# Performance work log

Measured on AMD Instinct MI355X. Metric: run time of the kernel, lower is better.

Reference implementation:

```python
import jax, jax.numpy as jnp
import numpy as np

N, D, H, C, L, G, E = 50000, 128, 128, 40, 3, 4, 800000
GRID = jnp.linspace(-2.0, 2.0, G)          # RBF grid on [-2, 2]
DENOM = 4.0 / (G - 1)                      # (grid_max - grid_min) / (num_grids - 1)


def _layernorm(x, g, b, eps=1e-5):
    m = x.mean(-1, keepdims=True)
    v = x.var(-1, keepdims=True)
    return (x - m) * jax.lax.rsqrt(v + eps) * g + b


def _fkan(x, ln_g, ln_b, sw, bw, bb):
    # FastKANLayer: layernorm -> Gaussian RBF basis -> bias-free spline linear, + silu base update
    xn = _layernorm(x, ln_g, ln_b)
    basis = jnp.exp(-(((xn[..., None] - GRID) / DENOM) ** 2))     # [n, d, G]
    ret = basis.reshape(x.shape[0], -1) @ sw.T                    # [n, out]
    return ret + jax.nn.silu(x) @ bw.T + bb


def _gcn_prop(h, src, dst, n):
    # symmetric GCN normalization with self-loops already appended to src/dst
    deg = jax.ops.segment_sum(jnp.ones(src.shape[0], h.dtype), dst, num_segments=n)
    dis = jnp.where(deg > 0, jax.lax.rsqrt(deg), 0.0)
    norm = dis[src] * dis[dst]                                    # [e]
    return jax.ops.segment_sum(h[src] * norm[:, None], dst, num_segments=n)


def _batchnorm(x, g, b, eps=1e-5):
    m = x.mean(0)
    v = x.var(0)  # biased variance, as torch BN uses for normalization
    return (x - m) * jax.lax.rsqrt(v + eps) * g + b


def setup_inputs() -> dict:
    key = jax.random.key(0)
    ks = jax.random.split(key, 8)
    x = jax.random.normal(ks[0], (N, D), jnp.float32)
    edge_index = jax.random.randint(ks[1], (2, E), 0, N, jnp.int64)
    return {
        "x": x,
        "edge_index": edge_index,
        "ln_g": jnp.ones((L, D), jnp.float32),
        "ln_b": jnp.zeros((L, D), jnp.float32),
        "sw": jax.random.normal(ks[2], (L, H, D * G), jnp.float32) * 0.1,
        "bw": jax.random.normal(ks[3], (L, H, D), jnp.float32) * (1.0 / np.sqrt(D)),
        "bb": jnp.zeros((L, H), jnp.float32),
        "gcn_bias": jnp.zeros((L, H), jnp.float32),
        "bn_g": jnp.ones((L, H), jnp.float32),
        "bn_b": jnp.zeros((L, H), jnp.float32),
        "ln_g_out": jnp.ones((D + L * H,), jnp.float32),
        "ln_b_out": jnp.zeros((D + L * H,), jnp.float32),
        "sw_out": jax.random.normal(ks[4], (C, (D + L * H) * G), jnp.float32) * 0.1,
        "bw_out": jax.random.normal(ks[5], (C, D + L * H), jnp.float32) * (1.0 / np.sqrt(D + L * H)),
        "bb_out": jnp.zeros((C,), jnp.float32),
    }


def reference(x, edge_index, ln_g, ln_b, sw, bw, bb, gcn_bias, bn_g, bn_b,
              ln_g_out, ln_b_out, sw_out, bw_out, bb_out):
    loops = jnp.arange(N, dtype=edge_index.dtype)
    src = jnp.concatenate([edge_index[0], loops])
    dst = jnp.concatenate([edge_index[1], loops])
    feats = [x]
    h = x
    for i in range(L):  # fixed small layer count
        h = _fkan(h, ln_g[i], ln_b[i], sw[i], bw[i], bb[i])
        h = _gcn_prop(h, src, dst, N) + gcn_bias[i]
        h = _batchnorm(h, bn_g[i], bn_b[i])
        feats.append(h)
    xcat = jnp.concatenate(feats, axis=1)  # [N, D + L*H] skip-concat
    return _fkan(xcat, ln_g_out, ln_b_out, sw_out, bw_out, bb_out)
```

## Files before the change

### kernel.cpp

```cpp
#include <hip/hip_runtime.h>
#include <hip/hip_bf16.h>

#define TPB 256
#define TPBO 512

typedef __attribute__((ext_vector_type(8))) short s8v;
typedef __attribute__((ext_vector_type(4))) float f32x4;
typedef unsigned short u16;

__device__ __forceinline__ u16 f2bf(float f){
  union { __hip_bfloat16 h; u16 u; } cv;
  cv.h = __float2bfloat16(f);
  return cv.u;
}

__device__ __forceinline__ unsigned pack_bf2(float lo, float hi){
  return (unsigned)f2bf(lo) | ((unsigned)f2bf(hi) << 16);
}

__device__ __forceinline__ float bflo(unsigned u){ return __uint_as_float(u << 16); }
__device__ __forceinline__ float bfhi(unsigned u){ return __uint_as_float(u & 0xffff0000u); }

__device__ __forceinline__ int wave_incl_scan(int v, int lane){
  #pragma unroll
  for (int off=1; off<64; off<<=1){
    int u = __shfl_up(v, off, 64);
    if (lane >= off) v += u;
  }
  return v;
}

__global__ __launch_bounds__(TPB) void count_k(const int* __restrict__ dstE, int* __restrict__ cnt, int E){
  int e = blockIdx.x*TPB + threadIdx.x;
  if (e < E) atomicAdd(&cnt[dstE[e]], 1);
}

__global__ __launch_bounds__(TPB) void scan1_k(const int* __restrict__ cnt, int* __restrict__ rowptr,
                                               int* __restrict__ bsum, float* __restrict__ disp, int nN){
  int t = threadIdx.x;
  int i = blockIdx.x*TPB + t;
  int lane = t & 63, wid = t >> 6;
  int v = (i < nN) ? cnt[i] : 0;
  if (i < nN) disp[i] = rsqrtf((float)v + 1.0f);
  int inc = wave_incl_scan(v, lane);
  __shared__ int wsum[4];
  if (lane == 63) wsum[wid] = inc;
  __syncthreads();
  int off = 0;
  #pragma unroll
  for (int w=0; w<4; ++w) if (w < wid) off += wsum[w];
  if (i < nN) rowptr[i] = inc - v + off;
  if (t == 0) bsum[blockIdx.x] = wsum[0]+wsum[1]+wsum[2]+wsum[3];
}

__global__ __launch_bounds__(TPB) void scan2_k(int* __restrict__ bsum, int nbk){
  int t = threadIdx.x;
  int lane = t & 63, wid = t >> 6;
  int v = (t < nbk) ? bsum[t] : 0;
  int inc = wave_incl_scan(v, lane);
  __shared__ int wsum[4];
  if (lane == 63) wsum[wid] = inc;
  __syncthreads();
  int off = 0;
  #pragma unroll
  for (int w=0; w<4; ++w) if (w < wid) off += wsum[w];
  __syncthreads();
  if (t < nbk) bsum[t] = inc - v + off;
}

__global__ __launch_bounds__(TPB) void scan3_k(int* __restrict__ rowptr, const int* __restrict__ bsum, int nN, int E){
  int i = blockIdx.x*TPB + threadIdx.x;
  if (i < nN) rowptr[i] += bsum[blockIdx.x];
  if (i == 0) rowptr[nN] = E;
}

__global__ __launch_bounds__(TPB) void fill_k(const int* __restrict__ srcE, const int* __restrict__ dstE,
                                              const int* __restrict__ rowptr, int* __restrict__ cursor,
                                              int* __restrict__ csr, int E){
  int e = blockIdx.x*TPB + threadIdx.x;
  if (e >= E) return;
  int d = dstE[e];
  int pos = atomicAdd(&cursor[d], 1);
  csr[rowptr[d] + pos] = srcE[e];
}

__global__ __launch_bounds__(TPB) void prep_wpre_k(const float* __restrict__ sw, const float* __restrict__ bw,
                                                   u16* __restrict__ wpre, int IN, int KSTEPS, int NTILES, int OUTW){
  int idx = blockIdx.x*TPB + threadIdx.x;
  if (idx >= NTILES*KSTEPS*512) return;
  int b = idx & 7, lane = (idx >> 3) & 63, rest = idx >> 9;
  int kstep = rest % KSTEPS, nt = rest / KSTEPS;
  int chunk = kstep / 5, g = kstep % 5;
  int d = chunk*32 + ((lane >> 4)*8 + b);
  int n = nt*16 + (lane & 15);
  float v = 0.f;
  if (n < OUTW) v = (g < 4) ? sw[(size_t)n*IN*4 + d*4 + g] : bw[(size_t)n*IN + d];
  wpre[idx] = f2bf(v);
}

__device__ __forceinline__ void build_frags(const float* __restrict__ h8, float mean, float rstd,
                                            const float* __restrict__ lngv, const float* __restrict__ lnbv,
                                            s8v* __restrict__ a){
  float bas[5][8];
  #pragma unroll
  for (int u=0; u<8; ++u){
    float v = h8[u];
    float xn = (v - mean)*rstd*lngv[u] + lnbv[u];
    float y = 0.900841806f*xn;
    float d0 = y + 1.80168361f;
    float d1 = y + 0.600561204f;
    float d2 = y - 0.600561204f;
    float d3 = y - 1.80168361f;
    bas[0][u] = __builtin_amdgcn_exp2f(-d0*d0);
    bas[1][u] = __builtin_amdgcn_exp2f(-d1*d1);
    bas[2][u] = __builtin_amdgcn_exp2f(-d2*d2);
    bas[3][u] = __builtin_amdgcn_exp2f(-d3*d3);
    float e = __builtin_amdgcn_exp2f(-1.44269504f*v);
    bas[4][u] = v * __builtin_amdgcn_rcpf(1.f + e);
  }
  #pragma unroll
  for (int g=0; g<5; ++g){
    #pragma unroll
    for (int j=0; j<4; ++j)
      ((unsigned*)&a[g])[j] = pack_bf2(bas[g][2*j], bas[g][2*j+1]);
  }
}

template<bool BF16IN>
__global__ __launch_bounds__(TPB) void fkan_layer_k(
    const float* __restrict__ in32, const u16* __restrict__ in16,
    const float* __restrict__ scsh,
    const float* __restrict__ lng, const float* __restrict__ lnb,
    const u16* __restrict__ wpre, const float* __restrict__ bias,
    const float* __restrict__ disp, u16* __restrict__ hs, int nN)
{
  const int t = threadIdx.x;
  const int wv = blockIdx.x*(TPB/64) + (t >> 6);
  const int ngrp = (nN + 15) >> 4;
  const int ng = wv >> 1, jh = wv & 1;
  if (ng >= ngrp) return;
  const int l = t & 63, clo = l & 15, kq = l >> 4;
  const int node = ng*16 + clo;
  const int nc = node < nN ? node : nN-1;

  float h[4][8];
  #pragma unroll
  for (int c=0; c<4; ++c){
    if (BF16IN){
      uint4 raw = *(const uint4*)(in16 + (size_t)nc*128 + c*32 + kq*8);
      h[c][0]=bflo(raw.x); h[c][1]=bfhi(raw.x);
      h[c][2]=bflo(raw.y); h[c][3]=bfhi(raw.y);
      h[c][4]=bflo(raw.z); h[c][5]=bfhi(raw.z);
      h[c][6]=bflo(raw.w); h[c][7]=bfhi(raw.w);
      #pragma unroll
      for (int u=0; u<8; ++u){
        int d = c*32 + kq*8 + u;
        h[c][u] = fmaf(h[c][u], scsh[d], scsh[128 + d]);
      }
    } else {
      const float* hrow = in32 + (size_t)nc*128;
      *(float4*)&h[c][0] = *(const float4*)(hrow + c*32 + kq*8);
      *(float4*)&h[c][4] = *(const float4*)(hrow + c*32 + kq*8 + 4);
    }
  }
  float s = 0.f, sq = 0.f;
  #pragma unroll
  for (int c=0; c<4; ++c)
    #pragma unroll
    for (int u=0; u<8; ++u){ float v = h[c][u]; s += v; sq += v*v; }
  s  += __shfl_xor(s, 16, 64);  s  += __shfl_xor(s, 32, 64);
  sq += __shfl_xor(sq, 16, 64); sq += __shfl_xor(sq, 32, 64);
  float mean = s * (1.f/128.f);
  float var  = fmaxf(sq * (1.f/128.f) - mean*mean, 0.f);
  float rstd = rsqrtf(var + 1e-5f);

  f32x4 acc[4];
  #pragma unroll
  for (int j=0; j<4; ++j) acc[j] = (f32x4)0.f;

  for (int c=0; c<4; ++c){
    float lngv[8], lnbv[8];
    *(float4*)&lngv[0] = *(const float4*)(lng + c*32 + kq*8);
    *(float4*)&lngv[4] = *(const float4*)(lng + c*32 + kq*8 + 4);
    *(float4*)&lnbv[0] = *(const float4*)(lnb + c*32 + kq*8);
    *(float4*)&lnbv[4] = *(const float4*)(lnb + c*32 + kq*8 + 4);
    s8v a[5];
    build_frags(h[c], mean, rstd, lngv, lnbv, a);
    #pragma unroll
    for (int ks=0; ks<5; ++ks){
      const int kglob = c*5 + ks;
      #pragma unroll
      for (int j=0; j<4; ++j){
        s8v b = *(const s8v*)(wpre + ((size_t)((jh*4 + j)*20 + kglob)*64 + l)*8);
        acc[j] = __builtin_amdgcn_mfma_f32_16x16x32_bf16(a[ks], b, acc[j], 0, 0, 0);
      }
    }
  }
  float bv[4];
  #pragma unroll
  for (int j=0; j<4; ++j) bv[j] = bias[(jh*4 + j)*16 + clo];
  #pragma unroll
  for (int rr=0; rr<4; ++rr){
    int nw = ng*16 + kq*4 + rr;
    if (nw < nN){
      float dsc = disp[nw];
      #pragma unroll
      for (int j=0; j<4; ++j)
        hs[(size_t)nw*128 + (jh*4 + j)*16 + clo] = f2bf((acc[j][rr] + bv[j]) * dsc);
    }
  }
}

__global__ __launch_bounds__(TPBO, 4) void fkan_out_k(
    const float* __restrict__ x, const u16* __restrict__ hl16,
    const float* __restrict__ scshAll,
    const float* __restrict__ lng, const float* __restrict__ lnb,
    const u16* __restrict__ wpre, const float* __restrict__ bias,
    float* __restrict__ out, int nN)
{
  __shared__ float sstat[8][16][4];
  __shared__ float sred[8][24][64];
  const int t = threadIdx.x;
  const int w = t >> 6, l = t & 63, clo = l & 15, kq = l >> 4;
  const int nb0 = blockIdx.x * 32;
  int nc0 = nb0 + clo;      nc0 = nc0 < nN ? nc0 : nN-1;
  int nc1 = nb0 + 16 + clo; nc1 = nc1 < nN ? nc1 : nN-1;

  float h0[2][8], h1[2][8];
  #pragma unroll
  for (int cc=0; cc<2; ++cc){
    const int c = w*2 + cc;
    const int d0 = c*32 + kq*8;
    if (d0 < 128){
      const float* s0 = x + (size_t)nc0*128 + d0;
      const float* s1 = x + (size_t)nc1*128 + d0;
      *(float4*)&h0[cc][0] = *(const float4*)(s0);  *(float4*)&h0[cc][4] = *(const float4*)(s0+4);
      *(float4*)&h1[cc][0] = *(const float4*)(s1);  *(float4*)&h1[cc][4] = *(const float4*)(s1+4);
    } else {
      int dd = d0 - 128, li = dd >> 7, cc2 = dd & 127;
      uint4 r0 = *(const uint4*)(hl16 + ((size_t)li*nN + nc0)*128 + cc2);
      uint4 r1 = *(const uint4*)(hl16 + ((size_t)li*nN + nc1)*128 + cc2);
      h0[cc][0]=bflo(r0.x); h0[cc][1]=bfhi(r0.x); h0[cc][2]=bflo(r0.y); h0[cc][3]=bfhi(r0.y);
      h0[cc][4]=bflo(r0.z); h0[cc][5]=bfhi(r0.z); h0[cc][6]=bflo(r0.w); h0[cc][7]=bfhi(r0.w);
      h1[cc][0]=bflo(r1.x); h1[cc][1]=bfhi(r1.x); h1[cc][2]=bflo(r1.y); h1[cc][3]=bfhi(r1.y);
      h1[cc][4]=bflo(r1.z); h1[cc][5]=bfhi(r1.z); h1[cc][6]=bflo(r1.w); h1[cc][7]=bfhi(r1.w);
      #pragma unroll
      for (int u=0; u<8; ++u){
        float sc = scshAll[li*256 + cc2 + u], sh = scshAll[li*256 + 128 + cc2 + u];
        h0[cc][u] = fmaf(h0[cc][u], sc, sh);
        h1[cc][u] = fmaf(h1[cc][u], sc, sh);
      }
    }
  }
  float s0=0.f, q0=0.f, s1=0.f, q1=0.f;
  #pragma unroll
  for (int cc=0; cc<2; ++cc)
    #pragma unroll
    for (int u=0; u<8; ++u){
      float a0v = h0[cc][u], a1v = h1[cc][u];
      s0 += a0v; q0 += a0v*a0v;
      s1 += a1v; q1 += a1v*a1v;
    }
  s0 += __shfl_xor(s0, 16, 64); s0 += __shfl_xor(s0, 32, 64);
  q0 += __shfl_xor(q0, 16, 64); q0 += __shfl_xor(q0, 32, 64);
  s1 += __shfl_xor(s1, 16, 64); s1 += __shfl_xor(s1, 32, 64);
  q1 += __shfl_xor(q1, 16, 64); q1 += __shfl_xor(q1, 32, 64);
  if (l < 16){
    sstat[w][clo][0] = s0; sstat[w][clo][1] = q0;
    sstat[w][clo][2] = s1; sstat[w][clo][3] = q1;
  }
  __syncthreads();
  float S0=0.f, Q0=0.f, S1=0.f, Q1=0.f;
  #pragma unroll
  for (int ww=0; ww<8; ++ww){
    S0 += sstat[ww][clo][0]; Q0 += sstat[ww][clo][1];
    S1 += sstat[ww][clo][2]; Q1 += sstat[ww][clo][3];
  }
  const float mean0 = S0 * (1.f/512.f);
  const float rstd0 = rsqrtf(fmaxf(Q0*(1.f/512.f) - mean0*mean0, 0.f) + 1e-5f);
  const float mean1 = S1 * (1.f/512.f);
  const float rstd1 = rsqrtf(fmaxf(Q1*(1.f/512.f) - mean1*mean1, 0.f) + 1e-5f);

  f32x4 acc[2][3];
  #pragma unroll
  for (int m=0; m<2; ++m)
    #pragma unroll
    for (int j=0; j<3; ++j) acc[m][j] = (f32x4)0.f;

  #pragma unroll
  for (int cc=0; cc<2; ++cc){
    const int c = w*2 + cc;
    const int d0 = c*32 + kq*8;
    float lngv[8], lnbv[8];
    *(float4*)&lngv[0] = *(const float4*)(lng + d0);
    *(float4*)&lngv[4] = *(const float4*)(lng + d0 + 4);
    *(float4*)&lnbv[0] = *(const float4*)(lnb + d0);
    *(float4*)&lnbv[4] = *(const float4*)(lnb + d0 + 4);
    s8v a0[5], a1[5];
    build_frags(h0[cc], mean0, rstd0, lngv, lnbv, a0);
    build_frags(h1[cc], mean1, rstd1, lngv, lnbv, a1);
    #pragma unroll
    for (int ks=0; ks<5; ++ks){
      const int kglob = c*5 + ks;
      #pragma unroll
      for (int j=0; j<3; ++j){
        s8v b = *(const s8v*)(wpre + ((size_t)(j*80 + kglob)*64 + l)*8);
        acc[0][j] = __builtin_amdgcn_mfma_f32_16x16x32_bf16(a0[ks], b, acc[0][j], 0, 0, 0);
        acc[1][j] = __builtin_amdgcn_mfma_f32_16x16x32_bf16(a1[ks], b, acc[1][j], 0, 0, 0);
      }
    }
  }
  #pragma unroll
  for (int m=0; m<2; ++m)
    #pragma unroll
    for (int j=0; j<3; ++j)
      #pragma unroll
      for (int rr=0; rr<4; ++rr)
        sred[w][m*12 + j*4 + rr][l] = acc[m][j][rr];
  __syncthreads();
  #pragma unroll
  for (int k=0; k<3; ++k){
    int q = t + k*TPBO;
    int slot = q >> 6, l2 = q & 63;
    float val = 0.f;
    #pragma unroll
    for (int ww=0; ww<8; ++ww) val += sred[ww][slot][l2];
    int m = slot >= 12 ? 1 : 0;
    int jrr = slot - m*12;
    int j = jrr >> 2, rr = jrr & 3;
    int nodeq = nb0 + m*16 + (l2 >> 4)*4 + rr;
    int col = j*16 + (l2 & 15);
    if (nodeq < nN && col < 40)
      out[(size_t)nodeq*40 + col] = val + bias[col];
  }
}

__device__ __forceinline__ void acc_bf8(uint4 u, float* __restrict__ a){
  a[0] += bflo(u.x); a[1] += bfhi(u.x);
  a[2] += bflo(u.y); a[3] += bfhi(u.y);
  a[4] += bflo(u.z); a[5] += bfhi(u.z);
  a[6] += bflo(u.w); a[7] += bfhi(u.w);
}

__global__ __launch_bounds__(TPB) void gcn_k(const u16* __restrict__ hs, const int* __restrict__ rowptr,
                                             const int* __restrict__ csr, const float* __restrict__ disp,
                                             u16* __restrict__ hl, int nN){
  int g = blockIdx.x*TPB + threadIdx.x;
  int wv = g >> 6, lane = g & 63;
  const int li = lane & 15, qd = lane >> 4;
  int n = wv*4 + qd;
  if (n >= nN) return;
  const uint4* H4 = (const uint4*)hs;
  int e0 = rowptr[n], e1 = rowptr[n+1];
  float a[8];
  #pragma unroll
  for (int j=0; j<8; ++j) a[j] = 0.f;
  for (int base = e0; base < e1; base += 4){
    int r[4];
    #pragma unroll
    for (int k=0; k<4; ++k){
      int idx = base + k;
      int idc = idx < e1 ? idx : e1-1;
      int rv  = csr[idc];
      r[k] = idx < e1 ? rv : nN;
    }
    #pragma unroll
    for (int k=0; k<4; ++k){
      uint4 u = H4[(size_t)r[k]*16 + li];
      acc_bf8(u, a);
    }
  }
  uint4 u = H4[(size_t)n*16 + li];
  acc_bf8(u, a);
  float dn = disp[n];
  uint4 o;
  o.x = pack_bf2(a[0]*dn, a[1]*dn);
  o.y = pack_bf2(a[2]*dn, a[3]*dn);
  o.z = pack_bf2(a[4]*dn, a[5]*dn);
  o.w = pack_bf2(a[6]*dn, a[7]*dn);
  *(uint4*)(hl + (size_t)n*128 + li*8) = o;
}

__global__ __launch_bounds__(TPB) void bn_stat_k(const u16* __restrict__ hl, float* __restrict__ stats, int nN){
  int cp   = threadIdx.x & 63;
  int strm = threadIdx.x >> 6;
  const unsigned* H = (const unsigned*)hl;
  float s0=0.f, s1=0.f, q0=0.f, q1=0.f;
  for (int r = blockIdx.x*4 + strm; r < nN; r += gridDim.x*4){
    unsigned u = H[(size_t)r*64 + cp];
    float lo = bflo(u), hi = bfhi(u);
    s0 += lo; q0 += lo*lo; s1 += hi; q1 += hi*hi;
  }
  __shared__ float ls[4][64][4];
  ls[strm][cp][0] = s0; ls[strm][cp][1] = q0; ls[strm][cp][2] = s1; ls[strm][cp][3] = q1;
  __syncthreads();
  if (strm == 0){
    float S0 = ls[0][cp][0]+ls[1][cp][0]+ls[2][cp][0]+ls[3][cp][0];
    float Q0 = ls[0][cp][1]+ls[1][cp][1]+ls[2][cp][1]+ls[3][cp][1];
    float S1 = ls[0][cp][2]+ls[1][cp][2]+ls[2][cp][2]+ls[3][cp][2];
    float Q1 = ls[0][cp][3]+ls[1][cp][3]+ls[2][cp][3]+ls[3][cp][3];
    atomicAdd(&stats[cp*2],       S0);
    atomicAdd(&stats[cp*2+1],     S1);
    atomicAdd(&stats[128+cp*2],   Q0);
    atomicAdd(&stats[128+cp*2+1], Q1);
  }
}

__global__ void bn_fin_k(float* __restrict__ stats, const float* __restrict__ g, const float* __restrict__ b,
                         float* __restrict__ scsh, int nN){
  int c = threadIdx.x;
  float inv = 1.f/(float)nN;
  float m = stats[c]*inv;
  float var = fmaxf(stats[128+c]*inv - m*m, 0.f);
  float sc = g[c]*rsqrtf(var + 1e-5f);
  scsh[c] = sc;
  scsh[128+c] = b[c] - m*sc;
  stats[c] = 0.f;
  stats[128+c] = 0.f;
}

extern "C" void kernel_launch(void* const* d_in, const int* in_sizes, int n_in,
                              void* d_out, int out_size, void* d_ws, size_t ws_size,
                              hipStream_t stream)
{
  const float* x        = (const float*)d_in[0];
  const int*   ei       = (const int*)d_in[1];
  const float* ln_g     = (const float*)d_in[2];
  const float* ln_b     = (const float*)d_in[3];
  const float* sw       = (const float*)d_in[4];
  const float* bw       = (const float*)d_in[5];
  const float* bb       = (const float*)d_in[6];
  const float* bn_g     = (const float*)d_in[8];
  const float* bn_b     = (const float*)d_in[9];
  const float* ln_g_out = (const float*)d_in[10];
  const float* ln_b_out = (const float*)d_in[11];
  const float* sw_out   = (const float*)d_in[12];
  const float* bw_out   = (const float*)d_in[13];
  const float* bb_out   = (const float*)d_in[14];
  float* out = (float*)d_out;

  const int nN = in_sizes[0] / 128;
  const int E  = in_sizes[1] / 2;

  char* ws = (char*)d_ws;
  size_t off = 0;
  auto alloc = [&](size_t bytes)->char*{
    char* p = ws + off; off = (off + bytes + 255) & ~size_t(255); return p;
  };
  u16*   hl16  = (u16*)alloc((size_t)3*nN*128*2);
  u16*   hs    = (u16*)alloc((size_t)(nN+1)*128*2);
  float* disp  = (float*)alloc((size_t)nN*4);
  float* stats = (float*)alloc(256*4);
  float* scshL = (float*)alloc(3*256*4);
  u16*   wpreL = (u16*)alloc((size_t)3*8*20*512*2);
  u16*   wpreO = (u16*)alloc((size_t)3*80*512*2);
  int* cnt     = (int*)alloc((size_t)nN*4);
  int* cursor  = (int*)alloc((size_t)nN*4);
  int* rowptr  = (int*)alloc((size_t)(nN+1)*4);
  int* bsum    = (int*)alloc(256*4);
  int* csr     = (int*)alloc((size_t)E*4);
  (void)ws_size; (void)n_in; (void)out_size;

  const int* srcE = ei;
  const int* dstE = ei + E;

  hipMemsetAsync(cnt, 0, (size_t)nN*4, stream);
  hipMemsetAsync(cursor, 0, (size_t)nN*4, stream);
  hipMemsetAsync(stats, 0, 256*4, stream);
  hipMemsetAsync(hs + (size_t)nN*128, 0, 256, stream);

  for (int i=0; i<3; ++i)
    prep_wpre_k<<<(8*20*512 + TPB-1)/TPB, TPB, 0, stream>>>(
        sw + (size_t)i*128*512, bw + (size_t)i*128*128, wpreL + (size_t)i*8*20*512, 128, 20, 8, 128);
  prep_wpre_k<<<(3*80*512 + TPB-1)/TPB, TPB, 0, stream>>>(
      sw_out, bw_out, wpreO, 512, 80, 3, 40);

  const int nbE = (E + TPB-1)/TPB;
  const int nbN = (nN + TPB-1)/TPB;
  count_k<<<nbE, TPB, 0, stream>>>(dstE, cnt, E);
  scan1_k<<<nbN, TPB, 0, stream>>>(cnt, rowptr, bsum, disp, nN);
  scan2_k<<<1, TPB, 0, stream>>>(bsum, nbN);
  scan3_k<<<nbN, TPB, 0, stream>>>(rowptr, bsum, nN, E);
  fill_k<<<nbE, TPB, 0, stream>>>(srcE, dstE, rowptr, cursor, csr, E);

  const int nbG = (((nN + 3)/4)*64 + TPB-1)/TPB;
  const int nbS = (nN*64 + TPB-1)/TPB;
  (void)nbS;
  const int nbL = (((nN + 15)/16)*2 + 3)/4;
  const int nbO = (nN + 31)/32;

  for (int i=0; i<3; ++i){
    if (i == 0){
      fkan_layer_k<false><<<nbL, TPB, 0, stream>>>(
          x, (const u16*)nullptr, (const float*)nullptr,
          ln_g, ln_b, wpreL, bb, disp, hs, nN);
    } else {
      fkan_layer_k<true><<<nbL, TPB, 0, stream>>>(
          (const float*)nullptr, hl16 + (size_t)(i-1)*nN*128, scshL + (size_t)(i-1)*256,
          ln_g + (size_t)i*128, ln_b + (size_t)i*128,
          wpreL + (size_t)i*8*20*512, bb + (size_t)i*128, disp, hs, nN);
    }
    gcn_k<<<nbG, TPB, 0, stream>>>(hs, rowptr, csr, disp, hl16 + (size_t)i*nN*128, nN);
    bn_stat_k<<<256, TPB, 0, stream>>>(hl16 + (size_t)i*nN*128, stats, nN);
    bn_fin_k<<<1, 128, 0, stream>>>(stats, bn_g + (size_t)i*128, bn_b + (size_t)i*128,
                                    scshL + (size_t)i*256, nN);
  }

  fkan_out_k<<<nbO, TPBO, 0, stream>>>(
      x, hl16, scshL, ln_g_out, ln_b_out, wpreO, bb_out, out, nN);
}
```

Before: 435.3 us.

## Fuse batchnorm statistics into GCN aggregation and store output reduction in half

The GCN gather kernel now uses a grid-stride loop over nodes with a fixed grid. Each thread accumulates per-channel sum and sum-of-squares of its outputs, reduces them in shared memory, then atomically adds them to global stats, which removes the separate bn_stat_k pass that re-read the aggregated features. Statistics are now taken from fp32 values before bf16 rounding. Separately, the output kernel's cross-wave reduction buffer is stored as fp16 instead of fp32, halving its LDS footprint at the cost of precision and possible overflow in the partial sums.

```diff
diff --git a/kernel.cpp b/kernel.cpp
--- a/kernel.cpp
+++ b/kernel.cpp
@@ -1,5 +1,6 @@
 #include <hip/hip_runtime.h>
 #include <hip/hip_bf16.h>
+#include <hip/hip_fp16.h>
 
 #define TPB 256
 #define TPBO 512
@@ -219,7 +220,7 @@
     float* __restrict__ out, int nN)
 {
   __shared__ float sstat[8][16][4];
-  __shared__ float sred[8][24][64];
+  __shared__ __half sred[8][24][64];
   const int t = threadIdx.x;
   const int w = t >> 6, l = t & 63, clo = l & 15, kq = l >> 4;
   const int nb0 = blockIdx.x * 32;
@@ -316,7 +317,7 @@
     for (int j=0; j<3; ++j)
       #pragma unroll
       for (int rr=0; rr<4; ++rr)
-        sred[w][m*12 + j*4 + rr][l] = acc[m][j][rr];
+        sred[w][m*12 + j*4 + rr][l] = __float2half(acc[m][j][rr]);
   __syncthreads();
   #pragma unroll
   for (int k=0; k<3; ++k){
@@ -324,7 +325,7 @@
     int slot = q >> 6, l2 = q & 63;
     float val = 0.f;
     #pragma unroll
-    for (int ww=0; ww<8; ++ww) val += sred[ww][slot][l2];
+    for (int ww=0; ww<8; ++ww) val += __half2float(sred[ww][slot][l2]);
     int m = slot >= 12 ? 1 : 0;
     int jrr = slot - m*12;
     int j = jrr >> 2, rr = jrr & 3;
@@ -344,66 +345,62 @@
 
 __global__ __launch_bounds__(TPB) void gcn_k(const u16* __restrict__ hs, const int* __restrict__ rowptr,
                                              const int* __restrict__ csr, const float* __restrict__ disp,
-                                             u16* __restrict__ hl, int nN){
-  int g = blockIdx.x*TPB + threadIdx.x;
-  int wv = g >> 6, lane = g & 63;
-  const int li = lane & 15, qd = lane >> 4;
-  int n = wv*4 + qd;
-  if (n >= nN) return;
+                                             u16* __restrict__ hl, float* __restrict__ stats, int nN){
+  __shared__ float lstat[256];
+  for (int i=threadIdx.x; i<256; i+=TPB) lstat[i] = 0.f;
+  __syncthreads();
+  const int li = threadIdx.x & 15;
+  const int tq0 = (blockIdx.x*TPB + threadIdx.x) >> 4;
+  const int qstride = (gridDim.x*TPB) >> 4;
   const uint4* H4 = (const uint4*)hs;
-  int e0 = rowptr[n], e1 = rowptr[n+1];
-  float a[8];
-  #pragma unroll
-  for (int j=0; j<8; ++j) a[j] = 0.f;
-  for (int base = e0; base < e1; base += 4){
-    int r[4];
-    #pragma unroll
-    for (int k=0; k<4; ++k){
-      int idx = base + k;
-      int idc = idx < e1 ? idx : e1-1;
-      int rv  = csr[idc];
-      r[k] = idx < e1 ? rv : nN;
-    }
-    #pragma unroll
-    for (int k=0; k<4; ++k){
-      uint4 u = H4[(size_t)r[k]*16 + li];
-      acc_bf8(u, a);
-    }
-  }
-  uint4 u = H4[(size_t)n*16 + li];
-  acc_bf8(u, a);
-  float dn = disp[n];
-  uint4 o;
-  o.x = pack_bf2(a[0]*dn, a[1]*dn);
-  o.y = pack_bf2(a[2]*dn, a[3]*dn);
-  o.z = pack_bf2(a[4]*dn, a[5]*dn);
-  o.w = pack_bf2(a[6]*dn, a[7]*dn);
-  *(uint4*)(hl + (size_t)n*128 + li*8) = o;
-}
-
-__global__ __launch_bounds__(TPB) void bn_stat_k(const u16* __restrict__ hl, float* __restrict__ stats, int nN){
-  int cp   = threadIdx.x & 63;
-  int strm = threadIdx.x >> 6;
-  const unsigned* H = (const unsigned*)hl;
-  float s0=0.f, s1=0.f, q0=0.f, q1=0.f;
-  for (int r = blockIdx.x*4 + strm; r < nN; r += gridDim.x*4){
-    unsigned u = H[(size_t)r*64 + cp];
-    float lo = bflo(u), hi = bfhi(u);
-    s0 += lo; q0 += lo*lo; s1 += hi; q1 += hi*hi;
-  }
-  __shared__ float ls[4][64][4];
-  ls[strm][cp][0] = s0; ls[strm][cp][1] = q0; ls[strm][cp][2] = s1; ls[strm][cp][3] = q1;
-  __syncthreads();
-  if (strm == 0){
-    float S0 = ls[0][cp][0]+ls[1][cp][0]+ls[2][cp][0]+ls[3][cp][0];
-    float Q0 = ls[0][cp][1]+ls[1][cp][1]+ls[2][cp][1]+ls[3][cp][1];
-    float S1 = ls[0][cp][2]+ls[1][cp][2]+ls[2][cp][2]+ls[3][cp][2];
-    float Q1 = ls[0][cp][3]+ls[1][cp][3]+ls[2][cp][3]+ls[3][cp][3];
-    atomicAdd(&stats[cp*2],       S0);
-    atomicAdd(&stats[cp*2+1],     S1);
-    atomicAdd(&stats[128+cp*2],   Q0);
-    atomicAdd(&stats[128+cp*2+1], Q1);
-  }
+  float bs[8], bq[8];
+  #pragma unroll
+  for (int j=0; j<8; ++j){ bs[j]=0.f; bq[j]=0.f; }
+
+  for (int n = tq0; n < nN; n += qstride){
+    int e0 = rowptr[n], e1 = rowptr[n+1];
+    float a[8];
+    #pragma unroll
+    for (int j=0; j<8; ++j) a[j] = 0.f;
+    for (int base = e0; base < e1; base += 4){
+      int r[4];
+      #pragma unroll
+      for (int k=0; k<4; ++k){
+        int idx = base + k;
+        int idc = idx < e1 ? idx : e1-1;
+        int rv  = csr[idc];
+        r[k] = idx < e1 ? rv : nN;
+      }
+      #pragma unroll
+      for (int k=0; k<4; ++k){
+        uint4 u = H4[(size_t)r[k]*16 + li];
+        acc_bf8(u, a);
+      }
+    }
+    uint4 u = H4[(size_t)n*16 + li];
+    acc_bf8(u, a);
+    float dn = disp[n];
+    #pragma unroll
+    for (int j=0; j<8; ++j){
+      float v = a[j]*dn;
+      a[j] = v;
+      bs[j] += v;
+      bq[j] += v*v;
+    }
+    uint4 o;
+    o.x = pack_bf2(a[0], a[1]);
+    o.y = pack_bf2(a[2], a[3]);
+    o.z = pack_bf2(a[4], a[5]);
+    o.w = pack_bf2(a[6], a[7]);
+    *(uint4*)(hl + (size_t)n*128 + li*8) = o;
+  }
+  #pragma unroll
+  for (int j=0; j<8; ++j){
+    atomicAdd(&lstat[li*8 + j], bs[j]);
+    atomicAdd(&lstat[128 + li*8 + j], bq[j]);
+  }
+  __syncthreads();
+  atomicAdd(&stats[threadIdx.x], lstat[threadIdx.x]);
 }
 
 __global__ void bn_fin_k(float* __restrict__ stats, const float* __restrict__ g, const float* __restrict__ b,
@@ -483,9 +480,7 @@
   scan3_k<<<nbN, TPB, 0, stream>>>(rowptr, bsum, nN, E);
   fill_k<<<nbE, TPB, 0, stream>>>(srcE, dstE, rowptr, cursor, csr, E);
 
-  const int nbG = (((nN + 3)/4)*64 + TPB-1)/TPB;
-  const int nbS = (nN*64 + TPB-1)/TPB;
-  (void)nbS;
+  const int nbG = 1024;
   const int nbL = (((nN + 15)/16)*2 + 3)/4;
   const int nbO = (nN + 31)/32;
 
@@ -500,8 +495,7 @@
           ln_g + (size_t)i*128, ln_b + (size_t)i*128,
           wpreL + (size_t)i*8*20*512, bb + (size_t)i*128, disp, hs, nN);
     }
-    gcn_k<<<nbG, TPB, 0, stream>>>(hs, rowptr, csr, disp, hl16 + (size_t)i*nN*128, nN);
-    bn_stat_k<<<256, TPB, 0, stream>>>(hl16 + (size_t)i*nN*128, stats, nN);
+    gcn_k<<<nbG, TPB, 0, stream>>>(hs, rowptr, csr, disp, hl16 + (size_t)i*nN*128, stats, nN);
     bn_fin_k<<<1, 128, 0, stream>>>(stats, bn_g + (size_t)i*128, bn_b + (size_t)i*128,
                                     scshL + (size_t)i*256, nN);
   }
```

Result: no change. 441.9 us (+1.5%).
